# Kernel optimization log

Measured on AMD Instinct MI355X. Metric: run time of the kernel, lower is better.

Reference implementation:

```python
import jax, jax.numpy as jnp
import numpy as np

D = 256; N_GRU = 4; L = 3; RATIO = 0.8; B = 64; PAD = 0
VOCAB = 50000; N = 20000; E = 320000; T = 16


def setup_inputs() -> dict:
    key = jax.random.key(0)
    ks = jax.random.split(key, 10)
    s = 0.05
    return {
        "x_tokens": jax.random.randint(ks[0], (N, T), 0, VOCAB),
        "edge_index": jax.random.randint(ks[1], (2, E), 0, N),
        "batch": jnp.sort(jax.random.randint(ks[2], (N,), 0, B)),
        "embed": jax.random.normal(ks[3], (VOCAB, D)) * s,
        "ggc_W": jax.random.normal(ks[4], (L, N_GRU, D, D)) * s,
        "gru_Wih": jax.random.normal(ks[5], (L, 3 * D, D)) * s,
        "gru_Whh": jax.random.normal(ks[6], (L, 3 * D, D)) * s,
        "gru_bih": jnp.zeros((L, 3 * D)),
        "gru_bhh": jnp.zeros((L, 3 * D)),
        "topk_p": jax.random.normal(ks[7], (L, D)) * s,
        "gate_W": jax.random.normal(ks[8], (D, 1)) * s,
        "gate_b": jnp.zeros((1,)),
    }


def gru_cell(m, h, Wih, Whh, bih, bhh):
    gi = m @ Wih.T + bih
    gh = h @ Whh.T + bhh
    i_r, i_z, i_n = jnp.split(gi, 3, axis=-1)
    h_r, h_z, h_n = jnp.split(gh, 3, axis=-1)
    r = jax.nn.sigmoid(i_r + h_r)
    z = jax.nn.sigmoid(i_z + h_z)
    n = jnp.tanh(i_n + r * h_n)
    return (1.0 - z) * n + z * h


def gated_graph_conv(h, src, dst, emask, W, Wih, Whh, bih, bhh):
    # PyG GatedGraphConv: per step, transform then scatter-add source->target, then GRU update
    for l in range(N_GRU):
        msg = (h @ W[l])[src] * emask[:, None]            # [E, D]
        agg = jax.ops.segment_sum(msg, dst, num_segments=h.shape[0])
        h = gru_cell(agg, h, Wih, Whh, bih, bhh)
    return h


def topk_pool(x, p, nmask, batch, src, dst, emask):
    # PyG TopKPooling: score = tanh(x.p/||p||), keep top ceil(ratio*n) per graph, x *= score
    score = jnp.tanh((x @ p) / jnp.linalg.norm(p))
    skey = jnp.where(nmask, score, -1e9)
    order = jnp.lexsort((-skey, batch))                   # by graph asc, score desc
    counts = jax.ops.segment_sum(jnp.ones((N,), jnp.int32), batch, num_segments=B)
    starts = jnp.cumsum(counts) - counts
    rank = jnp.zeros((N,), jnp.int32).at[order].set(
        jnp.arange(N, dtype=jnp.int32) - starts[batch[order]])
    n_valid = jax.ops.segment_sum(nmask.astype(jnp.int32), batch, num_segments=B)
    k = jnp.ceil(RATIO * n_valid.astype(jnp.float32)).astype(jnp.int32)
    keep = nmask & (rank < k[batch])
    x_new = jnp.where(keep[:, None], x * score[:, None], 0.0)
    emask_new = emask * keep[src].astype(emask.dtype) * keep[dst].astype(emask.dtype)
    return x_new, keep, emask_new


def global_att(x, nmask, batch, gW, gb):
    # GlobalAttention: segment softmax of Linear(x,1), weighted sum per graph
    logit = jnp.where(nmask, (x @ gW)[:, 0] + gb[0], -1e9)
    mx = jax.ops.segment_max(logit, batch, num_segments=B)
    e = jnp.where(nmask, jnp.exp(logit - mx[batch]), 0.0)
    denom = jax.ops.segment_sum(e, batch, num_segments=B)
    gate = e / jnp.maximum(denom[batch], 1e-12)
    return jax.ops.segment_sum(gate[:, None] * x, batch, num_segments=B)


def reference(x_tokens, edge_index, batch, embed, ggc_W, gru_Wih, gru_Whh,
              gru_bih, gru_bhh, topk_p, gate_W, gate_b):
    # STEncoder: embed token ids, mean-pool non-pad tokens per node
    tok_mask = (x_tokens != PAD)
    emb = embed[x_tokens] * tok_mask[..., None]
    h = emb.sum(1) / jnp.maximum(tok_mask.sum(1, keepdims=True), 1).astype(emb.dtype)
    src, dst = edge_index[0], edge_index[1]
    nmask = jnp.ones((N,), bool)
    emask = jnp.ones((E,), h.dtype)
    out = jnp.zeros((B, D), h.dtype)
    for l in range(L):
        h = jax.nn.relu(gated_graph_conv(h, src, dst, emask, ggc_W[l],
                                         gru_Wih[l], gru_Whh[l], gru_bih[l], gru_bhh[l]))
        h, nmask, emask = topk_pool(h, topk_p[l], nmask, batch, src, dst, emask)
        out = out + global_att(h, nmask, batch, gate_W, gate_b)
    return out
```

## Files before the change

kernel.cpp:

```cpp
#include <hip/hip_runtime.h>
#include <hip/hip_bf16.h>

namespace {

constexpr int NN = 20000;
constexpr int TT = 16;
constexpr int DD = 256;
constexpr int EE = 320000;
constexpr int BB = 64;
constexpr int NLAY = 3;
constexpr int NGRUS = 4;
constexpr int D3 = 768;
constexpr int NRB = 157;
constexpr int NXCD = 8;

typedef __bf16 bf16x8 __attribute__((ext_vector_type(8)));
typedef float  f32x4  __attribute__((ext_vector_type(4)));

__device__ __forceinline__ float us2f(unsigned short u){
  union { unsigned int i; float f; } v; v.i = ((unsigned int)u) << 16; return v.f;
}
__device__ __forceinline__ unsigned short f2us(float f){
  union { float f; unsigned int i; } v; v.f = f;
  unsigned int r = v.i + 0x7fff + ((v.i >> 16) & 1);
  return (unsigned short)(r >> 16);
}

__device__ __forceinline__ void gload16(const unsigned short* g, unsigned short* l){
  __builtin_amdgcn_global_load_lds(
      (const __attribute__((address_space(1))) unsigned int*)g,
      (__attribute__((address_space(3))) unsigned int*)l, 16, 0, 0);
}

__global__ void k_init(int* __restrict__ deg, int* __restrict__ cursor,
                       int* __restrict__ nmask, float* __restrict__ out){
  int i = blockIdx.x*256 + threadIdx.x;
  if (i < NN){ deg[i] = 0; cursor[i] = 0; nmask[i] = 1; }
  if (i < BB*DD) out[i] = 0.f;
}

__global__ void k_embed(const int* __restrict__ xt, const float* __restrict__ emb,
                        unsigned short* __restrict__ h){
  int wid = threadIdx.x >> 6, lane = threadIdx.x & 63;
  int n = blockIdx.x*4 + wid;
  if (n >= NN) return;
  int tk = (lane < TT) ? xt[n*TT + lane] : 0;
  float a0 = 0.f, a1 = 0.f, a2 = 0.f, a3 = 0.f;
  int cnt = 0;
  #pragma unroll
  for (int t = 0; t < TT; ++t){
    int tok = __shfl(tk, t);
    if (tok != 0){
      ++cnt;
      float4 v = *reinterpret_cast<const float4*>(emb + (size_t)tok*DD + lane*4);
      a0 += v.x; a1 += v.y; a2 += v.z; a3 += v.w;
    }
  }
  float inv = 1.f / (float)(cnt > 0 ? cnt : 1);
  ushort4 o;
  o.x = f2us(a0*inv); o.y = f2us(a1*inv); o.z = f2us(a2*inv); o.w = f2us(a3*inv);
  *reinterpret_cast<ushort4*>(h + (size_t)n*DD + lane*4) = o;
}

__global__ __launch_bounds__(256) void k_wf(const float* __restrict__ W,
                                            const float* __restrict__ Wih,
                                            unsigned short* __restrict__ WFThi,
                                            unsigned short* __restrict__ WFTlo){
  int lg = blockIdx.z; int l = lg / NGRUS;
  const float* A  = W   + (size_t)lg*DD*DD;
  const float* Bm = Wih + (size_t)l*D3*DD;
  unsigned short* oh = WFThi + (size_t)lg*D3*DD;
  unsigned short* ol = WFTlo + (size_t)lg*D3*DD;
  int k0 = blockIdx.y*64, j0 = blockIdx.x*64;
  __shared__ float sA[16][68], sB[16][68];
  int tid = threadIdx.x, ty = tid/16, tx = tid%16;
  float acc[4][4] = {};
  int m = tid >> 2, dg = (tid & 3)*4;
  for (int d0 = 0; d0 < DD; d0 += 16){
    float4 ua = *reinterpret_cast<const float4*>(A  + (size_t)(k0+m)*DD + d0+dg);
    float4 ub = *reinterpret_cast<const float4*>(Bm + (size_t)(j0+m)*DD + d0+dg);
    __syncthreads();
    sA[dg+0][m]=ua.x; sA[dg+1][m]=ua.y; sA[dg+2][m]=ua.z; sA[dg+3][m]=ua.w;
    sB[dg+0][m]=ub.x; sB[dg+1][m]=ub.y; sB[dg+2][m]=ub.z; sB[dg+3][m]=ub.w;
    __syncthreads();
    #pragma unroll
    for (int dd = 0; dd < 16; ++dd){
      float a[4], b[4];
      #pragma unroll
      for (int i=0;i<4;++i) a[i] = sA[dd][ty*4+i];
      #pragma unroll
      for (int j=0;j<4;++j) b[j] = sB[dd][tx*4+j];
      #pragma unroll
      for (int i=0;i<4;++i)
        #pragma unroll
        for (int j=0;j<4;++j) acc[i][j] += a[i]*b[j];
    }
  }
  for (int i=0;i<4;++i){
    int k = k0 + ty*4 + i;
    for (int j=0;j<4;++j){
      int c = j0 + tx*4 + j;
      float v = acc[i][j];
      unsigned short hi = f2us(v);
      float rem = v - us2f(hi);
      oh[(size_t)c*DD + k] = hi;
      ol[(size_t)c*DD + k] = f2us(rem);
    }
  }
}

__global__ void k_whh_split(const float* __restrict__ Whh, unsigned short* __restrict__ hi,
                            unsigned short* __restrict__ lo){
  size_t i = (size_t)blockIdx.x*256 + threadIdx.x;
  if (i >= (size_t)NLAY*D3*DD) return;
  float w = Whh[i];
  unsigned short h = f2us(w);
  hi[i] = h; lo[i] = f2us(w - us2f(h));
}

__global__ void k_deg(const int* __restrict__ dst, int* __restrict__ deg){
  int e = blockIdx.x*256 + threadIdx.x; if (e < EE) atomicAdd(&deg[dst[e]], 1);
}
__global__ void k_scan(const int* __restrict__ deg, int* __restrict__ offs){
  __shared__ int part[1024];
  int t = threadIdx.x; const int CH = 20;
  int base = t*CH; int s = 0;
  for (int i = 0; i < CH; ++i){ int idx = base+i; if (idx < NN) s += deg[idx]; }
  part[t] = s; __syncthreads();
  for (int o = 1; o < 1024; o <<= 1){
    int v = part[t]; int add = (t >= o) ? part[t-o] : 0;
    __syncthreads(); part[t] = v + add; __syncthreads();
  }
  int run = (t > 0) ? part[t-1] : 0;
  for (int i = 0; i < CH; ++i){ int idx = base+i; if (idx < NN){ offs[idx] = run; run += deg[idx]; } }
  if (t == 1023) offs[NN] = run;
}
__global__ void k_fill_csr(const int* __restrict__ src, const int* __restrict__ dst,
                           const int* __restrict__ offs, int* __restrict__ cursor,
                           int* __restrict__ csr_src){
  int e = blockIdx.x*256 + threadIdx.x; if (e >= EE) return;
  int d = dst[e]; int pos = atomicAdd(&cursor[d], 1);
  csr_src[offs[d] + pos] = src[e];
}

__global__ void k_bounds(const int* __restrict__ batch, int* __restrict__ starts65){
  int n = blockIdx.x*256 + threadIdx.x;
  if (n >= NN) return;
  int b = batch[n];
  int p = (n == 0) ? -1 : batch[n-1];
  for (int bb = p+1; bb <= b; ++bb) starts65[bb] = n;
  if (n == NN-1){
    for (int bb = b+1; bb <= BB; ++bb) starts65[bb] = NN;
  }
}
__global__ void k_cnts(const int* __restrict__ starts65, int* __restrict__ counts){
  int b = threadIdx.x;
  if (b < BB) counts[b] = starts65[b+1] - starts65[b];
}

__global__ void k_agg(const unsigned short* __restrict__ h, const int* __restrict__ offs,
                      const int* __restrict__ csr_src, unsigned short* __restrict__ agg){
  int wid = threadIdx.x >> 6, lane = threadIdx.x & 63;
  int n = blockIdx.x*4 + wid;
  if (n >= NN) return;
  int s = offs[n], e = offs[n+1];
  float a0 = 0.f, a1 = 0.f, a2 = 0.f, a3 = 0.f;
  for (int base = s; base < e; base += 64){
    int cnt = min(64, e - base);
    int idx = (lane < cnt) ? csr_src[base + lane] : 0;
    int i = 0;
    for (; i + 4 <= cnt; i += 4){
      int s0 = __shfl(idx, i+0), s1 = __shfl(idx, i+1);
      int s2 = __shfl(idx, i+2), s3 = __shfl(idx, i+3);
      ushort4 v0 = *reinterpret_cast<const ushort4*>(h + (size_t)s0*DD + lane*4);
      ushort4 v1 = *reinterpret_cast<const ushort4*>(h + (size_t)s1*DD + lane*4);
      ushort4 v2 = *reinterpret_cast<const ushort4*>(h + (size_t)s2*DD + lane*4);
      ushort4 v3 = *reinterpret_cast<const ushort4*>(h + (size_t)s3*DD + lane*4);
      a0 += us2f(v0.x); a1 += us2f(v0.y); a2 += us2f(v0.z); a3 += us2f(v0.w);
      a0 += us2f(v1.x); a1 += us2f(v1.y); a2 += us2f(v1.z); a3 += us2f(v1.w);
      a0 += us2f(v2.x); a1 += us2f(v2.y); a2 += us2f(v2.z); a3 += us2f(v2.w);
      a0 += us2f(v3.x); a1 += us2f(v3.y); a2 += us2f(v3.z); a3 += us2f(v3.w);
    }
    for (; i < cnt; ++i){
      int s0 = __shfl(idx, i);
      ushort4 v0 = *reinterpret_cast<const ushort4*>(h + (size_t)s0*DD + lane*4);
      a0 += us2f(v0.x); a1 += us2f(v0.y); a2 += us2f(v0.z); a3 += us2f(v0.w);
    }
  }
  ushort4 o;
  o.x = f2us(a0); o.y = f2us(a1); o.z = f2us(a2); o.w = f2us(a3);
  *reinterpret_cast<ushort4*>(agg + (size_t)n*DD + lane*4) = o;
}

__global__ __launch_bounds__(256, 4) void k_gru(
    const unsigned short* __restrict__ Ag, const unsigned short* __restrict__ Ah,
    const unsigned short* __restrict__ WfH, const unsigned short* __restrict__ WfL,
    const unsigned short* __restrict__ WhH, const unsigned short* __restrict__ WhL,
    const float* __restrict__ bih, const float* __restrict__ bhh,
    const int* __restrict__ nmask, unsigned short* __restrict__ Hn, int do_relu){
  __shared__ unsigned short sB[2][96*64];
  int t = threadIdx.x;
  int wv = t >> 6, lane = t & 63;
  int lr = lane & 15, kg = lane >> 4;

  int w = blockIdx.x;
  int q = (w & 7)*NRB + (w >> 3);
  int r0 = (q >> 3) * 128;
  int g0 = q & 7;

  int sw   = ((lane & 7) ^ (lane >> 3)) * 8;
  int rloc = lane >> 3;

  auto stageB = [&](int buf, int p){
    int a = p >> 1;
    const unsigned short* m = (p & 1) ? ((a & 4) ? WhL : WfL)
                                      : ((a & 4) ? WhH : WfH);
    int kin0 = (a & 3) * 64;
    #pragma unroll
    for (int i = 0; i < 3; ++i){
      int brow = (wv + i*4)*8;
      int gate = brow >> 5;
      int srcrow = gate*256 + g0*32 + (brow & 31) + rloc;
      gload16(m + (size_t)srcrow*DD + kin0 + sw, &sB[buf][brow*64]);
    }
  };

  f32x4 aR[2][2], aZ[2][2], aNi[2][2], aNh[2][2];
  #pragma unroll
  for (int rf = 0; rf < 2; ++rf)
    #pragma unroll
    for (int h2 = 0; h2 < 2; ++h2){
      aR[rf][h2] = (f32x4){0.f,0.f,0.f,0.f};  aZ[rf][h2] = (f32x4){0.f,0.f,0.f,0.f};
      aNi[rf][h2] = (f32x4){0.f,0.f,0.f,0.f}; aNh[rf][h2] = (f32x4){0.f,0.f,0.f,0.f};
    }

  size_t arow0 = (size_t)(r0 + wv*32 + lr) * DD;
  size_t arow1 = (size_t)(r0 + wv*32 + 16 + lr) * DD;

  bf16x8 aF0[2][2], aF1[2][2];
  #pragma unroll
  for (int kk2 = 0; kk2 < 2; ++kk2){
    aF0[0][kk2] = *reinterpret_cast<const bf16x8*>(Ag + arow0 + kk2*32 + kg*8);
    aF1[0][kk2] = *reinterpret_cast<const bf16x8*>(Ag + arow1 + kk2*32 + kg*8);
  }
  stageB(0, 0);

  #pragma unroll
  for (int a = 0; a < 8; ++a){
    int par = a & 1;
    int half = (a >> 2) & 1;
    #pragma unroll
    for (int ph = 0; ph < 2; ++ph){
      int p = a*2 + ph;
      int bbuf = p & 1;
      __syncthreads();
      if (p < 15) stageB(bbuf ^ 1, p + 1);
      if (ph == 0 && a < 7){
        const unsigned short* An = ((a+1) & 4) ? Ah : Ag;
        int kinn = ((a+1) & 3) * 64;
        #pragma unroll
        for (int kk2 = 0; kk2 < 2; ++kk2){
          aF0[par ^ 1][kk2] = *reinterpret_cast<const bf16x8*>(An + arow0 + kinn + kk2*32 + kg*8);
          aF1[par ^ 1][kk2] = *reinterpret_cast<const bf16x8*>(An + arow1 + kinn + kk2*32 + kg*8);
        }
      }
      __builtin_amdgcn_s_setprio(1);
      #pragma unroll
      for (int kk2 = 0; kk2 < 2; ++kk2){
        int cs = ((kk2*4 + kg) ^ (lr & 7)) * 8;
        bf16x8 a0 = aF0[par][kk2];
        bf16x8 a1 = aF1[par][kk2];
        #pragma unroll
        for (int h2 = 0; h2 < 2; ++h2){
          bf16x8 bR = *reinterpret_cast<const bf16x8*>(&sB[bbuf][(      h2*16 + lr)*64 + cs]);
          bf16x8 bZ = *reinterpret_cast<const bf16x8*>(&sB[bbuf][(32  + h2*16 + lr)*64 + cs]);
          bf16x8 bN = *reinterpret_cast<const bf16x8*>(&sB[bbuf][(64  + h2*16 + lr)*64 + cs]);
          aR[0][h2] = __builtin_amdgcn_mfma_f32_16x16x32_bf16(a0, bR, aR[0][h2], 0, 0, 0);
          aR[1][h2] = __builtin_amdgcn_mfma_f32_16x16x32_bf16(a1, bR, aR[1][h2], 0, 0, 0);
          aZ[0][h2] = __builtin_amdgcn_mfma_f32_16x16x32_bf16(a0, bZ, aZ[0][h2], 0, 0, 0);
          aZ[1][h2] = __builtin_amdgcn_mfma_f32_16x16x32_bf16(a1, bZ, aZ[1][h2], 0, 0, 0);
          if (half){
            aNh[0][h2] = __builtin_amdgcn_mfma_f32_16x16x32_bf16(a0, bN, aNh[0][h2], 0, 0, 0);
            aNh[1][h2] = __builtin_amdgcn_mfma_f32_16x16x32_bf16(a1, bN, aNh[1][h2], 0, 0, 0);
          } else {
            aNi[0][h2] = __builtin_amdgcn_mfma_f32_16x16x32_bf16(a0, bN, aNi[0][h2], 0, 0, 0);
            aNi[1][h2] = __builtin_amdgcn_mfma_f32_16x16x32_bf16(a1, bN, aNi[1][h2], 0, 0, 0);
          }
        }
      }
      __builtin_amdgcn_s_setprio(0);
    }
  }

  #pragma unroll
  for (int h2 = 0; h2 < 2; ++h2){
    int col = g0*32 + h2*16 + lr;
    float bRv = bih[col]       + bhh[col];
    float bZv = bih[256 + col] + bhh[256 + col];
    float bN1 = bih[512 + col];
    float bN2 = bhh[512 + col];
    #pragma unroll
    for (int rf = 0; rf < 2; ++rf){
      #pragma unroll
      for (int j = 0; j < 4; ++j){
        int row = r0 + wv*32 + rf*16 + kg*4 + j;
        if (row < NN){
          float r = 1.f/(1.f + expf(-(aR[rf][h2][j] + bRv)));
          float z = 1.f/(1.f + expf(-(aZ[rf][h2][j] + bZv)));
          float nv = tanhf(aNi[rf][h2][j] + bN1 + r*(aNh[rf][h2][j] + bN2));
          float ho = us2f(Ah[(size_t)row*DD + col]);
          float o = (1.f - z)*nv + z*ho;
          if (do_relu) o = fmaxf(o, 0.f);
          if (!nmask[row]) o = 0.f;
          Hn[(size_t)row*DD + col] = f2us(o);
        }
      }
    }
  }
}

__global__ void k_score(const unsigned short* __restrict__ h, const float* __restrict__ p,
                        float* __restrict__ score){
  int wid = threadIdx.x >> 6, lane = threadIdx.x & 63;
  int n = blockIdx.x*4 + wid; if (n >= NN) return;
  ushort4 hu = *reinterpret_cast<const ushort4*>(h + (size_t)n*DD + lane*4);
  float4 pv = *reinterpret_cast<const float4*>(p + lane*4);
  float dot = us2f(hu.x)*pv.x + us2f(hu.y)*pv.y + us2f(hu.z)*pv.z + us2f(hu.w)*pv.w;
  float pp = pv.x*pv.x + pv.y*pv.y + pv.z*pv.z + pv.w*pv.w;
  for (int o = 32; o; o >>= 1){ dot += __shfl_down(dot, o); pp += __shfl_down(pp, o); }
  if (lane == 0) score[n] = tanhf(dot / sqrtf(pp));
}

__global__ void k_topk(const float* __restrict__ score, const int* __restrict__ starts,
                       const int* __restrict__ counts, int* __restrict__ nmask){
  int b = blockIdx.x; int st = starts[b]; int cnt = min(counts[b], 1024);
  __shared__ float sc[1024]; __shared__ int ired[256];
  int t = threadIdx.x;
  int myvalid = 0;
  for (int i = t; i < cnt; i += 256){
    int node = st + i; int v = nmask[node];
    sc[i] = v ? score[node] : -1e30f;
    myvalid += v;
  }
  ired[t] = myvalid; __syncthreads();
  for (int o = 128; o; o >>= 1){ if (t < o) ired[t] += ired[t+o]; __syncthreads(); }
  int nv = ired[0];
  int k = (4*nv + 4)/5;
  __syncthreads();
  for (int i = t; i < cnt; i += 256){
    float si = sc[i]; int node = st + i; int keep = 0;
    if (si > -1e29f){
      int rank = 0;
      for (int j = 0; j < cnt; ++j){
        float sj = sc[j];
        rank += (sj > si) || (sj == si && j < i);
      }
      keep = (rank < k);
    }
    nmask[node] = keep;
  }
}

__global__ void k_scale(unsigned short* __restrict__ h, const float* __restrict__ score,
                        const int* __restrict__ nmask){
  int idx = blockIdx.x*256 + threadIdx.x;
  int n = idx >> 8;
  unsigned short v = nmask[n] ? f2us(us2f(h[idx])*score[n]) : (unsigned short)0;
  h[idx] = v;
}

__global__ void k_att(const unsigned short* __restrict__ h, const float* __restrict__ gW,
                      const float* __restrict__ gb, const int* __restrict__ starts,
                      const int* __restrict__ counts, const int* __restrict__ nmask,
                      float* __restrict__ outacc){
  int b = blockIdx.x; int st = starts[b]; int cnt = min(counts[b], 1024);
  __shared__ float lg[1024]; __shared__ float red[256];
  int t = threadIdx.x, wid = t >> 6, lane = t & 63;
  float gbv = gb[0];
  for (int i = wid; i < cnt; i += 4){
    int node = st + i;
    ushort4 hu = *reinterpret_cast<const ushort4*>(h + (size_t)node*DD + lane*4);
    float4 wv = *reinterpret_cast<const float4*>(gW + lane*4);
    float dot = us2f(hu.x)*wv.x + us2f(hu.y)*wv.y + us2f(hu.z)*wv.z + us2f(hu.w)*wv.w;
    for (int o = 32; o; o >>= 1) dot += __shfl_down(dot, o);
    if (lane == 0) lg[i] = nmask[node] ? dot + gbv : -1e30f;
  }
  __syncthreads();
  float mx = -1e30f;
  for (int i = t; i < cnt; i += 256) mx = fmaxf(mx, lg[i]);
  red[t] = mx; __syncthreads();
  for (int o = 128; o; o >>= 1){ if (t < o) red[t] = fmaxf(red[t], red[t+o]); __syncthreads(); }
  mx = red[0]; __syncthreads();
  float se = 0.f;
  for (int i = t; i < cnt; i += 256){
    float e = (lg[i] > -1e29f) ? expf(lg[i] - mx) : 0.f;
    lg[i] = e; se += e;
  }
  red[t] = se; __syncthreads();
  for (int o = 128; o; o >>= 1){ if (t < o) red[t] += red[t+o]; __syncthreads(); }
  float denom = fmaxf(red[0], 1e-12f);
  __syncthreads();
  float a0=0.f,a1=0.f,a2=0.f,a3=0.f;
  int i = 0;
  for (; i + 4 <= cnt; i += 4){
    a0 += lg[i+0]*us2f(h[(size_t)(st+i+0)*DD + t]);
    a1 += lg[i+1]*us2f(h[(size_t)(st+i+1)*DD + t]);
    a2 += lg[i+2]*us2f(h[(size_t)(st+i+2)*DD + t]);
    a3 += lg[i+3]*us2f(h[(size_t)(st+i+3)*DD + t]);
  }
  for (; i < cnt; ++i) a0 += lg[i]*us2f(h[(size_t)(st+i)*DD + t]);
  outacc[(size_t)b*DD + t] += (a0+a1+a2+a3)/denom;
}

}

extern "C" void kernel_launch(void* const* d_in, const int* in_sizes, int n_in,
                              void* d_out, int out_size, void* d_ws, size_t ws_size,
                              hipStream_t stream){
  const int*   x_tokens = (const int*)d_in[0];
  const int*   e_src    = (const int*)d_in[1];
  const int*   e_dst    = e_src + EE;
  const int*   batch    = (const int*)d_in[2];
  const float* embed    = (const float*)d_in[3];
  const float* ggcW     = (const float*)d_in[4];
  const float* gWih     = (const float*)d_in[5];
  const float* gWhh     = (const float*)d_in[6];
  const float* gbih     = (const float*)d_in[7];
  const float* gbhh     = (const float*)d_in[8];
  const float* topkp    = (const float*)d_in[9];
  const float* gateW    = (const float*)d_in[10];
  const float* gateb    = (const float*)d_in[11];
  (void)in_sizes; (void)n_in; (void)out_size;
  float* out = (float*)d_out;

  char* ws = (char*)d_ws;
  size_t off = 0;
  auto carve = [&](size_t bytes)->char*{
    char* p = ws + off;
    off += (bytes + 255) & ~(size_t)255;
    return p;
  };
  unsigned short* h0    = (unsigned short*)carve((size_t)NN*DD*2);
  unsigned short* h1    = (unsigned short*)carve((size_t)NN*DD*2);
  unsigned short* agg   = (unsigned short*)carve((size_t)NN*DD*2);
  unsigned short* WFThi = (unsigned short*)carve((size_t)NLAY*NGRUS*D3*DD*2);
  unsigned short* WFTlo = (unsigned short*)carve((size_t)NLAY*NGRUS*D3*DD*2);
  unsigned short* WhhHi = (unsigned short*)carve((size_t)NLAY*D3*DD*2);
  unsigned short* WhhLo = (unsigned short*)carve((size_t)NLAY*D3*DD*2);
  float* score   = (float*)carve((size_t)NN*4);
  int* nmask     = (int*)carve((size_t)NN*4);
  int* deg       = (int*)carve((size_t)NN*4);
  int* cursor    = (int*)carve((size_t)NN*4);
  int* offs      = (int*)carve((size_t)(NN+1)*4);
  int* csr_src   = (int*)carve((size_t)EE*4);
  int* counts    = (int*)carve((size_t)BB*4);
  int* starts    = (int*)carve((size_t)(BB+1)*4);
  if (off > ws_size) return;

  k_init<<<(NN+255)/256, 256, 0, stream>>>(deg, cursor, nmask, out);
  k_embed<<<(NN+3)/4, 256, 0, stream>>>(x_tokens, embed, h0);
  k_wf<<<dim3(D3/64, DD/64, NLAY*NGRUS), 256, 0, stream>>>(ggcW, gWih, WFThi, WFTlo);
  k_whh_split<<<(NLAY*D3*DD + 255)/256, 256, 0, stream>>>(gWhh, WhhHi, WhhLo);
  k_deg<<<(EE+255)/256, 256, 0, stream>>>(e_dst, deg);
  k_scan<<<1, 1024, 0, stream>>>(deg, offs);
  k_fill_csr<<<(EE+255)/256, 256, 0, stream>>>(e_src, e_dst, offs, cursor, csr_src);
  k_bounds<<<(NN+255)/256, 256, 0, stream>>>(batch, starts);
  k_cnts<<<1, 64, 0, stream>>>(starts, counts);

  unsigned short* hc = h0; unsigned short* hn = h1;
  for (int l = 0; l < NLAY; ++l){
    const unsigned short* WhHl = WhhHi + (size_t)l*D3*DD;
    const unsigned short* WhLl = WhhLo + (size_t)l*D3*DD;
    const float* bihl = gbih + (size_t)l*D3;
    const float* bhhl = gbhh + (size_t)l*D3;
    for (int g = 0; g < NGRUS; ++g){
      const unsigned short* WfHl = WFThi + (size_t)(l*NGRUS+g)*D3*DD;
      const unsigned short* WfLl = WFTlo + (size_t)(l*NGRUS+g)*D3*DD;
      k_agg<<<(NN+3)/4, 256, 0, stream>>>(hc, offs, csr_src, agg);
      k_gru<<<NRB*NXCD, 256, 0, stream>>>(agg, hc, WfHl, WfLl, WhHl, WhLl,
                                          bihl, bhhl, nmask, hn,
                                          (g == NGRUS-1) ? 1 : 0);
      unsigned short* tmp = hc; hc = hn; hn = tmp;
    }
    k_score<<<NN/4, 256, 0, stream>>>(hc, topkp + (size_t)l*DD, score);
    k_topk<<<BB, 256, 0, stream>>>(score, starts, counts, nmask);
    k_scale<<<NN, 256, 0, stream>>>(hc, score, nmask);
    k_att<<<BB, 256, 0, stream>>>(hc, gateW, gateb, starts, counts, nmask, out);
  }
}
```

Measured before the change: 1.234 ms.

## Fuse score, top-k, scale and attention pooling into one per-graph kernel

Merges the four per-layer pooling kernels (score, topk, scale, att) into one kernel with one block per graph, so scores and keep flags stay in shared memory instead of global buffers. This removes three launches per layer and the global score array. The cost is that scoring and scaling now run on only 64 blocks instead of grid-wide launches, which lowers parallelism for the memory-bound passes over h. It also changes a few details, such as zeroing scaled values via s==0 and reading keep flags from shared memory.

```diff
diff --git a/kernel.cpp b/kernel.cpp
--- a/kernel.cpp
+++ b/kernel.cpp
@@ -319,27 +319,38 @@
   }
 }
 
-__global__ void k_score(const unsigned short* __restrict__ h, const float* __restrict__ p,
-                        float* __restrict__ score){
-  int wid = threadIdx.x >> 6, lane = threadIdx.x & 63;
-  int n = blockIdx.x*4 + wid; if (n >= NN) return;
-  ushort4 hu = *reinterpret_cast<const ushort4*>(h + (size_t)n*DD + lane*4);
+__global__ __launch_bounds__(256) void k_pool(
+    unsigned short* __restrict__ h, const float* __restrict__ p,
+    const float* __restrict__ gW, const float* __restrict__ gb,
+    const int* __restrict__ starts, const int* __restrict__ counts,
+    int* __restrict__ nmask, float* __restrict__ outacc){
+  int b = blockIdx.x; int st = starts[b]; int cnt = min(counts[b], 1024);
+  __shared__ float sc[1024]; __shared__ int kp[1024];
+  __shared__ float red[256]; __shared__ int ired[256];
+  __shared__ float s_pnorm;
+  int t = threadIdx.x, wid = t >> 6, lane = t & 63;
+
   float4 pv = *reinterpret_cast<const float4*>(p + lane*4);
-  float dot = us2f(hu.x)*pv.x + us2f(hu.y)*pv.y + us2f(hu.z)*pv.z + us2f(hu.w)*pv.w;
-  float pp = pv.x*pv.x + pv.y*pv.y + pv.z*pv.z + pv.w*pv.w;
-  for (int o = 32; o; o >>= 1){ dot += __shfl_down(dot, o); pp += __shfl_down(pp, o); }
-  if (lane == 0) score[n] = tanhf(dot / sqrtf(pp));
-}
-
-__global__ void k_topk(const float* __restrict__ score, const int* __restrict__ starts,
-                       const int* __restrict__ counts, int* __restrict__ nmask){
-  int b = blockIdx.x; int st = starts[b]; int cnt = min(counts[b], 1024);
-  __shared__ float sc[1024]; __shared__ int ired[256];
-  int t = threadIdx.x;
+  {
+    float pp = pv.x*pv.x + pv.y*pv.y + pv.z*pv.z + pv.w*pv.w;
+    for (int o = 32; o; o >>= 1) pp += __shfl_down(pp, o);
+    if (t == 0) s_pnorm = sqrtf(pp);
+  }
+  for (int i = wid; i < cnt; i += 4){
+    int node = st + i;
+    ushort4 hu = *reinterpret_cast<const ushort4*>(h + (size_t)node*DD + lane*4);
+    float dot = us2f(hu.x)*pv.x + us2f(hu.y)*pv.y + us2f(hu.z)*pv.z + us2f(hu.w)*pv.w;
+    for (int o = 32; o; o >>= 1) dot += __shfl_down(dot, o);
+    if (lane == 0) sc[i] = dot;
+  }
+  __syncthreads();
+  float pnorm = s_pnorm;
+
   int myvalid = 0;
   for (int i = t; i < cnt; i += 256){
     int node = st + i; int v = nmask[node];
-    sc[i] = v ? score[node] : -1e30f;
+    float s = tanhf(sc[i] / pnorm);
+    sc[i] = v ? s : -1e30f;
     myvalid += v;
   }
   ired[t] = myvalid; __syncthreads();
@@ -347,6 +358,7 @@
   int nv = ired[0];
   int k = (4*nv + 4)/5;
   __syncthreads();
+
   for (int i = t; i < cnt; i += 256){
     float si = sc[i]; int node = st + i; int keep = 0;
     if (si > -1e29f){
@@ -357,44 +369,41 @@
       }
       keep = (rank < k);
     }
+    kp[i] = keep;
     nmask[node] = keep;
   }
-}
-
-__global__ void k_scale(unsigned short* __restrict__ h, const float* __restrict__ score,
-                        const int* __restrict__ nmask){
-  int idx = blockIdx.x*256 + threadIdx.x;
-  int n = idx >> 8;
-  unsigned short v = nmask[n] ? f2us(us2f(h[idx])*score[n]) : (unsigned short)0;
-  h[idx] = v;
-}
-
-__global__ void k_att(const unsigned short* __restrict__ h, const float* __restrict__ gW,
-                      const float* __restrict__ gb, const int* __restrict__ starts,
-                      const int* __restrict__ counts, const int* __restrict__ nmask,
-                      float* __restrict__ outacc){
-  int b = blockIdx.x; int st = starts[b]; int cnt = min(counts[b], 1024);
-  __shared__ float lg[1024]; __shared__ float red[256];
-  int t = threadIdx.x, wid = t >> 6, lane = t & 63;
+  __syncthreads();
+
+  for (int i = t; i < cnt; i += 256)
+    if (!kp[i]) sc[i] = 0.f;
+  __syncthreads();
+
+  for (int i = 0; i < cnt; ++i){
+    size_t idx = (size_t)(st + i)*DD + t;
+    float s = sc[i];
+    h[idx] = (s == 0.f) ? (unsigned short)0 : f2us(us2f(h[idx])*s);
+  }
+  __syncthreads();
+
+  float4 wv4 = *reinterpret_cast<const float4*>(gW + lane*4);
   float gbv = gb[0];
   for (int i = wid; i < cnt; i += 4){
     int node = st + i;
     ushort4 hu = *reinterpret_cast<const ushort4*>(h + (size_t)node*DD + lane*4);
-    float4 wv = *reinterpret_cast<const float4*>(gW + lane*4);
-    float dot = us2f(hu.x)*wv.x + us2f(hu.y)*wv.y + us2f(hu.z)*wv.z + us2f(hu.w)*wv.w;
+    float dot = us2f(hu.x)*wv4.x + us2f(hu.y)*wv4.y + us2f(hu.z)*wv4.z + us2f(hu.w)*wv4.w;
     for (int o = 32; o; o >>= 1) dot += __shfl_down(dot, o);
-    if (lane == 0) lg[i] = nmask[node] ? dot + gbv : -1e30f;
+    if (lane == 0) sc[i] = kp[i] ? dot + gbv : -1e30f;
   }
   __syncthreads();
   float mx = -1e30f;
-  for (int i = t; i < cnt; i += 256) mx = fmaxf(mx, lg[i]);
+  for (int i = t; i < cnt; i += 256) mx = fmaxf(mx, sc[i]);
   red[t] = mx; __syncthreads();
   for (int o = 128; o; o >>= 1){ if (t < o) red[t] = fmaxf(red[t], red[t+o]); __syncthreads(); }
   mx = red[0]; __syncthreads();
   float se = 0.f;
   for (int i = t; i < cnt; i += 256){
-    float e = (lg[i] > -1e29f) ? expf(lg[i] - mx) : 0.f;
-    lg[i] = e; se += e;
+    float e = (sc[i] > -1e29f) ? expf(sc[i] - mx) : 0.f;
+    sc[i] = e; se += e;
   }
   red[t] = se; __syncthreads();
   for (int o = 128; o; o >>= 1){ if (t < o) red[t] += red[t+o]; __syncthreads(); }
@@ -403,12 +412,12 @@
   float a0=0.f,a1=0.f,a2=0.f,a3=0.f;
   int i = 0;
   for (; i + 4 <= cnt; i += 4){
-    a0 += lg[i+0]*us2f(h[(size_t)(st+i+0)*DD + t]);
-    a1 += lg[i+1]*us2f(h[(size_t)(st+i+1)*DD + t]);
-    a2 += lg[i+2]*us2f(h[(size_t)(st+i+2)*DD + t]);
-    a3 += lg[i+3]*us2f(h[(size_t)(st+i+3)*DD + t]);
-  }
-  for (; i < cnt; ++i) a0 += lg[i]*us2f(h[(size_t)(st+i)*DD + t]);
+    a0 += sc[i+0]*us2f(h[(size_t)(st+i+0)*DD + t]);
+    a1 += sc[i+1]*us2f(h[(size_t)(st+i+1)*DD + t]);
+    a2 += sc[i+2]*us2f(h[(size_t)(st+i+2)*DD + t]);
+    a3 += sc[i+3]*us2f(h[(size_t)(st+i+3)*DD + t]);
+  }
+  for (; i < cnt; ++i) a0 += sc[i]*us2f(h[(size_t)(st+i)*DD + t]);
   outacc[(size_t)b*DD + t] += (a0+a1+a2+a3)/denom;
 }
 
@@ -447,7 +456,6 @@
   unsigned short* WFTlo = (unsigned short*)carve((size_t)NLAY*NGRUS*D3*DD*2);
   unsigned short* WhhHi = (unsigned short*)carve((size_t)NLAY*D3*DD*2);
   unsigned short* WhhLo = (unsigned short*)carve((size_t)NLAY*D3*DD*2);
-  float* score   = (float*)carve((size_t)NN*4);
   int* nmask     = (int*)carve((size_t)NN*4);
   int* deg       = (int*)carve((size_t)NN*4);
   int* cursor    = (int*)carve((size_t)NN*4);
@@ -482,9 +490,7 @@
                                           (g == NGRUS-1) ? 1 : 0);
       unsigned short* tmp = hc; hc = hn; hn = tmp;
     }
-    k_score<<<NN/4, 256, 0, stream>>>(hc, topkp + (size_t)l*DD, score);
-    k_topk<<<BB, 256, 0, stream>>>(score, starts, counts, nmask);
-    k_scale<<<NN, 256, 0, stream>>>(hc, score, nmask);
-    k_att<<<BB, 256, 0, stream>>>(hc, gateW, gateb, starts, counts, nmask, out);
-  }
-}
+    k_pool<<<BB, 256, 0, stream>>>(hc, topkp + (size_t)l*DD, gateW, gateb,
+                                   starts, counts, nmask, out);
+  }
+}
```

Measured after the change: 1.359 ms. 1.1x slower.
